# Kernel tuning notes

Measured on AMD Instinct MI355X. Metric: run time of the kernel, lower is better.

Reference implementation:

```python
import jax, jax.numpy as jnp
import numpy as np

NUM_HEADS = 8
EMBED_DIM = 128
TOTAL_TOKENS = 32768  # must be divisible by NUM_HEADS; per-head seq = 4096


def setup_inputs() -> dict:
    key = jax.random.key(0)
    ks = jax.random.split(key, 7)
    E, H, T = EMBED_DIM, NUM_HEADS, TOTAL_TOKENS
    return {
        "query": jax.random.normal(ks[0], (T, E), dtype=jnp.float32),
        "key": jax.random.normal(ks[1], (T, E), dtype=jnp.float32),    # unused by the module
        "value": jax.random.normal(ks[2], (T, E), dtype=jnp.float32),  # unused by the module
        "W_qkv": jax.random.normal(ks[3], (E, 3 * E), dtype=jnp.float32) * (1.0 / np.sqrt(E)),
        "b_qkv": jax.random.normal(ks[4], (3 * E,), dtype=jnp.float32) * 0.02,
        "u_bias": jax.random.normal(ks[5], (H, E), dtype=jnp.float32) * 0.02,
        "v_bias": jax.random.normal(ks[6], (H, E), dtype=jnp.float32) * 0.02,
    }


def reference(query, key, value, W_qkv, b_qkv, u_bias, v_bias):
    H, E = NUM_HEADS, EMBED_DIM
    # Fused QKV projection (torch Linear: x @ W; W stored [in, 3*out] here)
    qkv = query @ W_qkv + b_qkv                      # [T, 3E]
    q, k, v = jnp.split(qkv, 3, axis=-1)             # each [T, E]

    def heads(x):
        # view(-1, H, E).transpose(0, 1): token axis is split across heads
        return jnp.swapaxes(x.reshape(-1, H, E), 0, 1)  # [H, S, E], S = T // H

    q = heads(q) + u_bias[:, None, :]                # per-head additive bias on q
    k = heads(k) + v_bias[:, None, :]                # per-head additive bias on k
    v = heads(v)

    scale = 1.0 / jnp.sqrt(jnp.asarray(E, dtype=q.dtype))
    scores = jnp.einsum('hse,hte->hst', q, k) * scale  # [H, S, S]
    attn = jax.nn.softmax(scores, axis=-1)
    return jnp.einsum('hst,hte->hse', attn, v)         # [H, S, E]
```

## Files before the change

kernel.cpp:

```cpp
#include <hip/hip_runtime.h>
#include <hip/hip_bf16.h>
#include <stdint.h>

#define NHEADS 8
#define SEQ    4096
#define DIM    128
#define TOK    32768

typedef __attribute__((ext_vector_type(4)))  float  f32x4;
typedef __attribute__((ext_vector_type(16))) float  f32x16;
typedef __attribute__((ext_vector_type(8)))  short  bf16x8;
typedef __attribute__((ext_vector_type(8)))  unsigned short u16x8;
typedef __attribute__((ext_vector_type(4)))  unsigned int   u32x4;

__device__ __forceinline__ unsigned short f32_to_bf16(float f) {
  union { float f; unsigned int u; } cv; cv.f = f;
  unsigned int u = cv.u;
  u += 0x7FFFu + ((u >> 16) & 1u);
  return (unsigned short)(u >> 16);
}
__device__ __forceinline__ unsigned cvtpk(float lo, float hi) {
  unsigned r;
  asm("v_cvt_pk_bf16_f32 %0, %1, %2" : "=v"(r) : "v"(lo), "v"(hi));
  return r;
}

__global__ __launch_bounds__(256) void wt_prep_kernel(
    const float* __restrict__ W, unsigned short* __restrict__ Wt) {
  const int tid = threadIdx.x;
  const int j  = blockIdx.x * 32 + (tid >> 3);
  const int k0 = (tid & 7) * 16;
  u16x8 a, b;
  #pragma unroll
  for (int x = 0; x < 8; ++x) a[x] = f32_to_bf16(W[(size_t)(k0 + x) * 384 + j]);
  #pragma unroll
  for (int x = 0; x < 8; ++x) b[x] = f32_to_bf16(W[(size_t)(k0 + 8 + x) * 384 + j]);
  *reinterpret_cast<u16x8*>(Wt + (size_t)j * 128 + k0)     = a;
  *reinterpret_cast<u16x8*>(Wt + (size_t)j * 128 + k0 + 8) = b;
}

__global__ __launch_bounds__(256, 2) void qkv_proj_kernel(
    const float* __restrict__ qin, const unsigned short* __restrict__ Wt,
    const float* __restrict__ bqkv, const float* __restrict__ ubias,
    const float* __restrict__ vbias,
    unsigned short* __restrict__ Qh, unsigned short* __restrict__ Kh,
    unsigned short* __restrict__ Vh) {
  __shared__ __align__(16) char Xl[16384];

  const int tid  = threadIdx.x;
  const int lane = tid & 63;
  const int w    = tid >> 6;
  const int wm   = w & 1;
  const int wn   = w >> 1;
  const int col  = lane & 31;
  const int hi   = lane >> 5;
  const int tok0 = blockIdx.x * 64;

  #pragma unroll
  for (int c = 0; c < 4; ++c) {
    int idx = tid + c * 256;
    int row = idx >> 4, c16 = idx & 15;
    const float* src = qin + (size_t)(tok0 + row) * DIM + c16 * 8;
    f32x4 lo  = *reinterpret_cast<const f32x4*>(src);
    f32x4 hi4 = *reinterpret_cast<const f32x4*>(src + 4);
    u32x4 pk;
    pk[0] = cvtpk(lo[0],  lo[1]);  pk[1] = cvtpk(lo[2],  lo[3]);
    pk[2] = cvtpk(hi4[0], hi4[1]); pk[3] = cvtpk(hi4[2], hi4[3]);
    *reinterpret_cast<u32x4*>(Xl + ((row * 256 + c16 * 16) ^ ((row & 7) << 4))) = pk;
  }
  __syncthreads();

  bf16x8 af[8];
  {
    int row = wm * 32 + col;
    #pragma unroll
    for (int kk = 0; kk < 8; ++kk)
      af[kk] = *reinterpret_cast<const bf16x8*>(
          Xl + ((row * 256 + kk * 32 + hi * 16) ^ ((row & 7) << 4)));
  }

  const int s0 = blockIdx.x * 8 + wm * 4;
  const float scale = 0.1275174309f;

  #pragma unroll
  for (int nt = 0; nt < 6; ++nt) {
    const int j0 = wn * 192 + nt * 32;

    const unsigned short* wp = Wt + (size_t)(j0 + col) * 128 + hi * 8;
    f32x16 acc = (f32x16)(0.0f);
    #pragma unroll
    for (int kk = 0; kk < 8; ++kk) {
      bf16x8 bf = *reinterpret_cast<const bf16x8*>(wp + kk * 16);
      acc = __builtin_amdgcn_mfma_f32_32x32x16_bf16(af[kk], bf, acc, 0, 0, 0);
    }

    const float bqv = bqkv[j0 + col];
    if (j0 < 128) {
      const int e = j0 + col;
      float ub[4];
      #pragma unroll
      for (int r = 0; r < 4; ++r) ub[r] = ubias[(r + 4 * hi) * DIM + e];
      #pragma unroll
      for (int i = 0; i < 16; ++i) {
        int h = (i & 3) + 4 * hi;
        Qh[((size_t)h * SEQ + s0 + (i >> 2)) * DIM + e] =
            f32_to_bf16((acc[i] + bqv + ub[i & 3]) * scale);
      }
    } else if (j0 < 256) {
      const int e = j0 - 128 + col;
      float vb[4];
      #pragma unroll
      for (int r = 0; r < 4; ++r) vb[r] = vbias[(r + 4 * hi) * DIM + e];
      #pragma unroll
      for (int i = 0; i < 16; ++i) {
        int h = (i & 3) + 4 * hi;
        Kh[((size_t)h * SEQ + s0 + (i >> 2)) * DIM + e] =
            f32_to_bf16(acc[i] + bqv + vb[i & 3]);
      }
    } else {
      const int e = j0 - 256 + col;
      #pragma unroll
      for (int i = 0; i < 16; ++i) {
        int h = (i & 3) + 4 * hi;
        Vh[((size_t)h * SEQ + s0 + (i >> 2)) * DIM + e] =
            f32_to_bf16(acc[i] + bqv);
      }
    }
  }
}

__global__ __launch_bounds__(256) void v_transpose_kernel(
    const unsigned short* __restrict__ Vh, unsigned short* __restrict__ Vt) {
  __shared__ unsigned short tile[64][66];
  const int h   = blockIdx.z;
  const int st  = blockIdx.y;
  const int et  = blockIdx.x;
  const int tid = threadIdx.x;

  #pragma unroll
  for (int c = 0; c < 2; ++c) {
    int idx = tid + c * 256;
    int sl  = idx >> 3;
    int e8  = idx & 7;
    u16x8 v = *reinterpret_cast<const u16x8*>(
        Vh + ((size_t)h * SEQ + st * 64 + sl) * DIM + et * 64 + e8 * 8);
    #pragma unroll
    for (int j = 0; j < 8; ++j) tile[sl][e8 * 8 + j] = v[j];
  }
  __syncthreads();
  #pragma unroll
  for (int c = 0; c < 2; ++c) {
    int idx = tid + c * 256;
    int el  = idx >> 3;
    int s8  = idx & 7;
    u16x8 v;
    #pragma unroll
    for (int j = 0; j < 8; ++j) v[j] = tile[s8 * 8 + j][el];
    *reinterpret_cast<u16x8*>(
        Vt + ((size_t)h * DIM + et * 64 + el) * SEQ + st * 64 + s8 * 8) = v;
  }
}

__global__ __launch_bounds__(256, 2) void attn_fwd_kernel(
    const unsigned short* __restrict__ Qh, const unsigned short* __restrict__ Kh,
    const unsigned short* __restrict__ Vt, float* __restrict__ Out) {
  __shared__ __align__(16) char smem[75008];
  float* lbuf = reinterpret_cast<float*>(smem + 73728);
  float* linv = reinterpret_cast<float*>(smem + 74752);

  const int tid  = threadIdx.x;
  const int lane = tid & 63;
  const int w    = tid >> 6;
  const int g    = w >> 1;
  const int wq   = w & 1;
  const int gtid = tid & 127;
  const int col  = lane & 31;
  const int hi   = lane >> 5;
  const int h    = blockIdx.x & 7;
  const int qb   = blockIdx.x >> 3;
  const int q0   = qb * 64 + wq * 32;

  bf16x8 qf[8];
  const unsigned short* qp = Qh + ((size_t)h * SEQ + q0 + col) * DIM + hi * 8;
  #pragma unroll
  for (int kk = 0; kk < 8; ++kk)
    qf[kk] = *reinterpret_cast<const bf16x8*>(qp + kk * 16);

  f32x16 acc[4];
  #pragma unroll
  for (int nt = 0; nt < 4; ++nt) acc[nt] = (f32x16)(0.0f);
  float l_r = 0.0f;

  const unsigned short* Kbase =
      Kh + (size_t)h * SEQ * DIM + (size_t)g * 2048 * DIM;
  const unsigned short* Vbase =
      Vt + (size_t)h * DIM * SEQ + (size_t)g * 2048;

  char* Kg = smem + g * 16384;
  char* Vg = smem + 32768 + g * 20480;

  bf16x8 kr[4], vr[4];

  auto load_tile = [&](int t) {
    #pragma unroll
    for (int c = 0; c < 4; ++c) {
      int idx = gtid + c * 128;
      int row = idx >> 4, c16 = idx & 15;
      kr[c] = *reinterpret_cast<const bf16x8*>(
          Kbase + (size_t)(t * 32 + row) * DIM + c16 * 8);
    }
    #pragma unroll
    for (int c = 0; c < 4; ++c) {
      int idx = gtid + c * 128;
      int e = idx >> 2, c8 = idx & 3;
      vr[c] = *reinterpret_cast<const bf16x8*>(
          Vbase + (size_t)e * SEQ + t * 32 + c8 * 8);
    }
  };
  auto write_tile = [&](int buf) {
    char* KB = Kg + buf * 8192;
    char* VB = Vg + buf * 10240;
    #pragma unroll
    for (int c = 0; c < 4; ++c) {
      int idx = gtid + c * 128;
      int row = idx >> 4, c16 = idx & 15;
      *reinterpret_cast<bf16x8*>(KB + ((row * 256 + c16 * 16) ^ ((row & 7) << 4))) = kr[c];
    }
    #pragma unroll
    for (int c = 0; c < 4; ++c) {
      int idx = gtid + c * 128;
      int e = idx >> 2, c8 = idx & 3;
      *reinterpret_cast<bf16x8*>(VB + (e * 80 + c8 * 16)) = vr[c];
    }
  };

  load_tile(0);
  write_tile(0);
  __syncthreads();

  for (int t = 0; t < 64; ++t) {
    const int cur = t & 1;
    if (t < 63) load_tile(t + 1);

    const char* KB = Kg + cur * 8192;
    const char* VB = Vg + cur * 10240;

    f32x16 sc0 = (f32x16)(0.0f);
    __builtin_amdgcn_s_setprio(1);
    #pragma unroll
    for (int kk = 0; kk < 8; ++kk) {
      bf16x8 kf = *reinterpret_cast<const bf16x8*>(
          KB + ((col * 256 + kk * 32 + hi * 16) ^ ((col & 7) << 4)));
      sc0 = __builtin_amdgcn_mfma_f32_32x32x16_bf16(kf, qf[kk], sc0, 0, 0, 0);
    }
    __builtin_amdgcn_s_setprio(0);

    bf16x8 vf0[2], vf1[2], vf2[2], vf3[2];
    #pragma unroll
    for (int ks = 0; ks < 2; ++ks) {
      vf0[ks] = *reinterpret_cast<const bf16x8*>(VB + ((col) * 80 + ks * 32 + hi * 16));
      vf1[ks] = *reinterpret_cast<const bf16x8*>(VB + ((32 + col) * 80 + ks * 32 + hi * 16));
      vf2[ks] = *reinterpret_cast<const bf16x8*>(VB + ((64 + col) * 80 + ks * 32 + hi * 16));
      vf3[ks] = *reinterpret_cast<const bf16x8*>(VB + ((96 + col) * 80 + ks * 32 + hi * 16));
    }

    float p[16];
    #pragma unroll
    for (int i = 0; i < 16; ++i) {
      p[i] = exp2f(sc0[i] - 16.0f);
      l_r += p[i];
    }
    bf16x8 pa[2];
    #pragma unroll
    for (int s16 = 0; s16 < 2; ++s16) {
      const float* p8 = &p[s16 * 8];
      unsigned A = cvtpk(p8[0], p8[1]);
      unsigned B = cvtpk(p8[4], p8[5]);
      asm("v_permlane32_swap_b32 %0, %1" : "+v"(A), "+v"(B));
      unsigned C = cvtpk(p8[2], p8[3]);
      unsigned D = cvtpk(p8[6], p8[7]);
      asm("v_permlane32_swap_b32 %0, %1" : "+v"(C), "+v"(D));
      u32x4 wd; wd[0] = A; wd[1] = C; wd[2] = B; wd[3] = D;
      pa[s16] = *reinterpret_cast<bf16x8*>(&wd);
    }

    __builtin_amdgcn_s_setprio(1);
    #pragma unroll
    for (int ks = 0; ks < 2; ++ks) {
      acc[0] = __builtin_amdgcn_mfma_f32_32x32x16_bf16(pa[ks], vf0[ks], acc[0], 0, 0, 0);
      acc[1] = __builtin_amdgcn_mfma_f32_32x32x16_bf16(pa[ks], vf1[ks], acc[1], 0, 0, 0);
      acc[2] = __builtin_amdgcn_mfma_f32_32x32x16_bf16(pa[ks], vf2[ks], acc[2], 0, 0, 0);
      acc[3] = __builtin_amdgcn_mfma_f32_32x32x16_bf16(pa[ks], vf3[ks], acc[3], 0, 0, 0);
    }
    __builtin_amdgcn_s_setprio(0);

    if (t < 63) write_tile(cur ^ 1);
    __syncthreads();
  }

  lbuf[w * 64 + lane] = l_r;
  if (g == 1) {
    char* mb = smem + wq * 16384;
    #pragma unroll
    for (int nt = 0; nt < 4; ++nt)
      #pragma unroll
      for (int i = 0; i < 4; ++i) {
        f32x4 v;
        v[0] = acc[nt][4 * i + 0]; v[1] = acc[nt][4 * i + 1];
        v[2] = acc[nt][4 * i + 2]; v[3] = acc[nt][4 * i + 3];
        *reinterpret_cast<f32x4*>(mb + (nt * 4 + i) * 1024 + lane * 16) = v;
      }
  }
  __syncthreads();
  if (g == 0) {
    const char* mb = smem + wq * 16384;
    #pragma unroll
    for (int nt = 0; nt < 4; ++nt)
      #pragma unroll
      for (int i = 0; i < 4; ++i) {
        f32x4 v = *reinterpret_cast<const f32x4*>(mb + (nt * 4 + i) * 1024 + lane * 16);
        acc[nt][4 * i + 0] += v[0]; acc[nt][4 * i + 1] += v[1];
        acc[nt][4 * i + 2] += v[2]; acc[nt][4 * i + 3] += v[3];
      }
    float ltot = lbuf[wq * 64 + col] + lbuf[wq * 64 + col + 32] +
                 lbuf[(wq + 2) * 64 + col] + lbuf[(wq + 2) * 64 + col + 32];
    linv[wq * 32 + col] = 1.0f / ltot;
    asm volatile("s_waitcnt lgkmcnt(0)" ::: "memory");

    float* op = Out + ((size_t)h * SEQ + q0) * DIM + col;
    #pragma unroll
    for (int g2 = 0; g2 < 4; ++g2) {
      f32x4 iv = *reinterpret_cast<f32x4*>(&linv[wq * 32 + 8 * g2 + 4 * hi]);
      #pragma unroll
      for (int nt = 0; nt < 4; ++nt)
        #pragma unroll
        for (int i = 0; i < 4; ++i)
          op[(size_t)(8 * g2 + 4 * hi + i) * DIM + nt * 32] =
              acc[nt][4 * g2 + i] * iv[i];
    }
  }
}

extern "C" void kernel_launch(void* const* d_in, const int* in_sizes, int n_in,
                              void* d_out, int out_size, void* d_ws, size_t ws_size,
                              hipStream_t stream) {
  (void)in_sizes; (void)n_in; (void)out_size; (void)ws_size;
  const float* query = (const float*)d_in[0];
  const float* W_qkv = (const float*)d_in[3];
  const float* b_qkv = (const float*)d_in[4];
  const float* u_bias = (const float*)d_in[5];
  const float* v_bias = (const float*)d_in[6];
  float* out = (float*)d_out;

  const size_t per = (size_t)NHEADS * SEQ * DIM;
  unsigned short* Qh = (unsigned short*)d_ws;
  unsigned short* Kh = Qh + per;
  unsigned short* Vh = Kh + per;
  unsigned short* Vt = Vh + per;
  unsigned short* Wt = Vt;

  wt_prep_kernel<<<dim3(12), dim3(256), 0, stream>>>(W_qkv, Wt);
  qkv_proj_kernel<<<dim3(TOK / 64), dim3(256), 0, stream>>>(
      query, Wt, b_qkv, u_bias, v_bias, Qh, Kh, Vh);
  v_transpose_kernel<<<dim3(2, 64, 8), dim3(256), 0, stream>>>(Vh, Vt);
  attn_fwd_kernel<<<dim3(NHEADS * 64), dim3(256), 0, stream>>>(Qh, Kh, Vt, out);
}
```

Baseline: 139.1 us.

## Use direct global-to-LDS loads and 12-wave blocks with 3-way KV split

The attention kernel now uses 768-thread blocks: 4 query waves (128 queries per block) times 3 KV groups that split the sequence into 43/43/42 tiles. K/V tiles are copied with global_load_lds, which removes the register staging and LDS write pass of the old prefetch. The PV MFMAs are split into two halves to lower register pressure. This brings a 3-way reduction through shared memory, 256 blocks on 256 CUs with one block per CU, and about 134KB of LDS per block. The launch bound of 768 threads with 3 blocks per CU is not reachable with that much LDS.

```diff
diff --git a/kernel.cpp b/kernel.cpp
--- a/kernel.cpp
+++ b/kernel.cpp
@@ -23,6 +23,11 @@
   unsigned r;
   asm("v_cvt_pk_bf16_f32 %0, %1, %2" : "=v"(r) : "v"(lo), "v"(hi));
   return r;
+}
+__device__ __forceinline__ void gload16(const void* g, void* l) {
+  __builtin_amdgcn_global_load_lds(
+      (const __attribute__((address_space(1))) unsigned int*)g,
+      (__attribute__((address_space(3))) unsigned int*)l, 16, 0, 0);
 }
 
 __global__ __launch_bounds__(256) void wt_prep_kernel(
@@ -161,24 +166,29 @@
   }
 }
 
-__global__ __launch_bounds__(256, 2) void attn_fwd_kernel(
+__global__ __launch_bounds__(768, 3) void attn_fwd_kernel(
     const unsigned short* __restrict__ Qh, const unsigned short* __restrict__ Kh,
     const unsigned short* __restrict__ Vt, float* __restrict__ Out) {
-  __shared__ __align__(16) char smem[75008];
-  float* lbuf = reinterpret_cast<float*>(smem + 73728);
-  float* linv = reinterpret_cast<float*>(smem + 74752);
+  __shared__ __align__(16) char smem[134656];
+  float* lbuf = reinterpret_cast<float*>(smem + 131072);
+  float* linv = reinterpret_cast<float*>(smem + 134144);
 
   const int tid  = threadIdx.x;
   const int lane = tid & 63;
   const int w    = tid >> 6;
-  const int g    = w >> 1;
-  const int wq   = w & 1;
-  const int gtid = tid & 127;
+  const int g    = w >> 2;
+  const int wq   = w & 3;
   const int col  = lane & 31;
   const int hi   = lane >> 5;
   const int h    = blockIdx.x & 7;
   const int qb   = blockIdx.x >> 3;
-  const int q0   = qb * 64 + wq * 32;
+  const int q0   = qb * 128 + wq * 32;
+
+  const int tbase = g * 43;
+  const int nt    = (g == 2) ? 42 : 43;
+
+  char* Kg = smem + g * 16384;
+  char* Vg = smem + 49152 + g * 20480;
 
   bf16x8 qf[8];
   const unsigned short* qp = Qh + ((size_t)h * SEQ + q0 + col) * DIM + hi * 8;
@@ -188,142 +198,144 @@
 
   f32x16 acc[4];
   #pragma unroll
-  for (int nt = 0; nt < 4; ++nt) acc[nt] = (f32x16)(0.0f);
+  for (int n = 0; n < 4; ++n) acc[n] = (f32x16)(0.0f);
   float l_r = 0.0f;
 
-  const unsigned short* Kbase =
-      Kh + (size_t)h * SEQ * DIM + (size_t)g * 2048 * DIM;
-  const unsigned short* Vbase =
-      Vt + (size_t)h * DIM * SEQ + (size_t)g * 2048;
-
-  char* Kg = smem + g * 16384;
-  char* Vg = smem + 32768 + g * 20480;
-
-  bf16x8 kr[4], vr[4];
-
-  auto load_tile = [&](int t) {
-    #pragma unroll
-    for (int c = 0; c < 4; ++c) {
-      int idx = gtid + c * 128;
-      int row = idx >> 4, c16 = idx & 15;
-      kr[c] = *reinterpret_cast<const bf16x8*>(
-          Kbase + (size_t)(t * 32 + row) * DIM + c16 * 8);
-    }
-    #pragma unroll
-    for (int c = 0; c < 4; ++c) {
-      int idx = gtid + c * 128;
-      int e = idx >> 2, c8 = idx & 3;
-      vr[c] = *reinterpret_cast<const bf16x8*>(
-          Vbase + (size_t)e * SEQ + t * 32 + c8 * 8);
+  int kofs[2];
+  #pragma unroll
+  for (int c2 = 0; c2 < 2; ++c2) {
+    int c   = wq * 2 + c2;
+    int row = c * 4 + (lane >> 4);
+    kofs[c2] = row * 256 + ((((lane & 15) ^ (row & 7)) << 4));
+  }
+  int vofs[3];
+  #pragma unroll
+  for (int c2 = 0; c2 < 3; ++c2) {
+    int c     = wq + 4 * c2;
+    int laddr = c * 1024 + lane * 16;
+    int row   = laddr / 80;
+    int unit  = (laddr - row * 80) >> 4;
+    vofs[c2]  = row * (SEQ * 2) + (unit < 4 ? unit * 16 : 0);
+  }
+
+  const char* KbaseB = reinterpret_cast<const char*>(Kh + (size_t)h * SEQ * DIM);
+  const char* VbaseB = reinterpret_cast<const char*>(Vt + (size_t)h * DIM * SEQ);
+
+  auto stage = [&](int tl, int buf) {
+    const char* ks = KbaseB + (size_t)(tbase + tl) * 8192;
+    #pragma unroll
+    for (int c2 = 0; c2 < 2; ++c2)
+      gload16(ks + kofs[c2], Kg + buf * 8192 + (wq * 2 + c2) * 1024);
+    const char* vs = VbaseB + (size_t)(tbase + tl) * 64;
+    #pragma unroll
+    for (int c2 = 0; c2 < 3; ++c2) {
+      int c = wq + 4 * c2;
+      if (c < 10)
+        gload16(vs + vofs[c2], Vg + buf * 10240 + c * 1024);
     }
   };
-  auto write_tile = [&](int buf) {
-    char* KB = Kg + buf * 8192;
-    char* VB = Vg + buf * 10240;
-    #pragma unroll
-    for (int c = 0; c < 4; ++c) {
-      int idx = gtid + c * 128;
-      int row = idx >> 4, c16 = idx & 15;
-      *reinterpret_cast<bf16x8*>(KB + ((row * 256 + c16 * 16) ^ ((row & 7) << 4))) = kr[c];
-    }
-    #pragma unroll
-    for (int c = 0; c < 4; ++c) {
-      int idx = gtid + c * 128;
-      int e = idx >> 2, c8 = idx & 3;
-      *reinterpret_cast<bf16x8*>(VB + (e * 80 + c8 * 16)) = vr[c];
-    }
-  };
-
-  load_tile(0);
-  write_tile(0);
+
+  stage(0, 0);
   __syncthreads();
 
-  for (int t = 0; t < 64; ++t) {
-    const int cur = t & 1;
-    if (t < 63) load_tile(t + 1);
-
-    const char* KB = Kg + cur * 8192;
-    const char* VB = Vg + cur * 10240;
-
-    f32x16 sc0 = (f32x16)(0.0f);
-    __builtin_amdgcn_s_setprio(1);
-    #pragma unroll
-    for (int kk = 0; kk < 8; ++kk) {
-      bf16x8 kf = *reinterpret_cast<const bf16x8*>(
-          KB + ((col * 256 + kk * 32 + hi * 16) ^ ((col & 7) << 4)));
-      sc0 = __builtin_amdgcn_mfma_f32_32x32x16_bf16(kf, qf[kk], sc0, 0, 0, 0);
-    }
-    __builtin_amdgcn_s_setprio(0);
-
-    bf16x8 vf0[2], vf1[2], vf2[2], vf3[2];
-    #pragma unroll
-    for (int ks = 0; ks < 2; ++ks) {
-      vf0[ks] = *reinterpret_cast<const bf16x8*>(VB + ((col) * 80 + ks * 32 + hi * 16));
-      vf1[ks] = *reinterpret_cast<const bf16x8*>(VB + ((32 + col) * 80 + ks * 32 + hi * 16));
-      vf2[ks] = *reinterpret_cast<const bf16x8*>(VB + ((64 + col) * 80 + ks * 32 + hi * 16));
-      vf3[ks] = *reinterpret_cast<const bf16x8*>(VB + ((96 + col) * 80 + ks * 32 + hi * 16));
-    }
-
-    float p[16];
-    #pragma unroll
-    for (int i = 0; i < 16; ++i) {
-      p[i] = exp2f(sc0[i] - 16.0f);
-      l_r += p[i];
-    }
-    bf16x8 pa[2];
-    #pragma unroll
-    for (int s16 = 0; s16 < 2; ++s16) {
-      const float* p8 = &p[s16 * 8];
-      unsigned A = cvtpk(p8[0], p8[1]);
-      unsigned B = cvtpk(p8[4], p8[5]);
-      asm("v_permlane32_swap_b32 %0, %1" : "+v"(A), "+v"(B));
-      unsigned C = cvtpk(p8[2], p8[3]);
-      unsigned D = cvtpk(p8[6], p8[7]);
-      asm("v_permlane32_swap_b32 %0, %1" : "+v"(C), "+v"(D));
-      u32x4 wd; wd[0] = A; wd[1] = C; wd[2] = B; wd[3] = D;
-      pa[s16] = *reinterpret_cast<bf16x8*>(&wd);
-    }
-
-    __builtin_amdgcn_s_setprio(1);
-    #pragma unroll
-    for (int ks = 0; ks < 2; ++ks) {
-      acc[0] = __builtin_amdgcn_mfma_f32_32x32x16_bf16(pa[ks], vf0[ks], acc[0], 0, 0, 0);
-      acc[1] = __builtin_amdgcn_mfma_f32_32x32x16_bf16(pa[ks], vf1[ks], acc[1], 0, 0, 0);
-      acc[2] = __builtin_amdgcn_mfma_f32_32x32x16_bf16(pa[ks], vf2[ks], acc[2], 0, 0, 0);
-      acc[3] = __builtin_amdgcn_mfma_f32_32x32x16_bf16(pa[ks], vf3[ks], acc[3], 0, 0, 0);
-    }
-    __builtin_amdgcn_s_setprio(0);
-
-    if (t < 63) write_tile(cur ^ 1);
+  for (int tl = 0; tl < 43; ++tl) {
+    const int cur = tl & 1;
+    if (tl + 1 < nt) stage(tl + 1, cur ^ 1);
+
+    if (tl < nt) {
+      const char* KB = Kg + cur * 8192;
+      const char* VB = Vg + cur * 10240;
+
+      f32x16 sc = (f32x16)(0.0f);
+      __builtin_amdgcn_s_setprio(1);
+      #pragma unroll
+      for (int kk = 0; kk < 8; ++kk) {
+        bf16x8 kf = *reinterpret_cast<const bf16x8*>(
+            KB + ((col * 256 + kk * 32 + hi * 16) ^ ((col & 7) << 4)));
+        sc = __builtin_amdgcn_mfma_f32_32x32x16_bf16(kf, qf[kk], sc, 0, 0, 0);
+      }
+      __builtin_amdgcn_s_setprio(0);
+
+      bf16x8 pa[2];
+      #pragma unroll
+      for (int s16 = 0; s16 < 2; ++s16) {
+        float p8[8];
+        #pragma unroll
+        for (int i = 0; i < 8; ++i) {
+          p8[i] = exp2f(sc[s16 * 8 + i] - 16.0f);
+          l_r += p8[i];
+        }
+        unsigned A = cvtpk(p8[0], p8[1]);
+        unsigned B = cvtpk(p8[4], p8[5]);
+        asm("v_permlane32_swap_b32 %0, %1" : "+v"(A), "+v"(B));
+        unsigned C = cvtpk(p8[2], p8[3]);
+        unsigned D = cvtpk(p8[6], p8[7]);
+        asm("v_permlane32_swap_b32 %0, %1" : "+v"(C), "+v"(D));
+        u32x4 wd; wd[0] = A; wd[1] = C; wd[2] = B; wd[3] = D;
+        pa[s16] = *reinterpret_cast<bf16x8*>(&wd);
+      }
+
+      bf16x8 vf0[2], vf1[2];
+      #pragma unroll
+      for (int ks = 0; ks < 2; ++ks) {
+        vf0[ks] = *reinterpret_cast<const bf16x8*>(VB + (col) * 80 + ks * 32 + hi * 16);
+        vf1[ks] = *reinterpret_cast<const bf16x8*>(VB + (32 + col) * 80 + ks * 32 + hi * 16);
+      }
+      __builtin_amdgcn_s_setprio(1);
+      #pragma unroll
+      for (int ks = 0; ks < 2; ++ks) {
+        acc[0] = __builtin_amdgcn_mfma_f32_32x32x16_bf16(pa[ks], vf0[ks], acc[0], 0, 0, 0);
+        acc[1] = __builtin_amdgcn_mfma_f32_32x32x16_bf16(pa[ks], vf1[ks], acc[1], 0, 0, 0);
+      }
+      __builtin_amdgcn_s_setprio(0);
+      #pragma unroll
+      for (int ks = 0; ks < 2; ++ks) {
+        vf0[ks] = *reinterpret_cast<const bf16x8*>(VB + (64 + col) * 80 + ks * 32 + hi * 16);
+        vf1[ks] = *reinterpret_cast<const bf16x8*>(VB + (96 + col) * 80 + ks * 32 + hi * 16);
+      }
+      __builtin_amdgcn_s_setprio(1);
+      #pragma unroll
+      for (int ks = 0; ks < 2; ++ks) {
+        acc[2] = __builtin_amdgcn_mfma_f32_32x32x16_bf16(pa[ks], vf0[ks], acc[2], 0, 0, 0);
+        acc[3] = __builtin_amdgcn_mfma_f32_32x32x16_bf16(pa[ks], vf1[ks], acc[3], 0, 0, 0);
+      }
+      __builtin_amdgcn_s_setprio(0);
+    }
+
     __syncthreads();
   }
 
   lbuf[w * 64 + lane] = l_r;
-  if (g == 1) {
-    char* mb = smem + wq * 16384;
-    #pragma unroll
-    for (int nt = 0; nt < 4; ++nt)
+  if (g > 0) {
+    char* mb = smem + ((g - 1) * 4 + wq) * 16384;
+    #pragma unroll
+    for (int n = 0; n < 4; ++n)
       #pragma unroll
       for (int i = 0; i < 4; ++i) {
         f32x4 v;
-        v[0] = acc[nt][4 * i + 0]; v[1] = acc[nt][4 * i + 1];
-        v[2] = acc[nt][4 * i + 2]; v[3] = acc[nt][4 * i + 3];
-        *reinterpret_cast<f32x4*>(mb + (nt * 4 + i) * 1024 + lane * 16) = v;
+        v[0] = acc[n][4 * i + 0]; v[1] = acc[n][4 * i + 1];
+        v[2] = acc[n][4 * i + 2]; v[3] = acc[n][4 * i + 3];
+        *reinterpret_cast<f32x4*>(mb + (n * 4 + i) * 1024 + lane * 16) = v;
       }
   }
   __syncthreads();
   if (g == 0) {
-    const char* mb = smem + wq * 16384;
-    #pragma unroll
-    for (int nt = 0; nt < 4; ++nt)
-      #pragma unroll
-      for (int i = 0; i < 4; ++i) {
-        f32x4 v = *reinterpret_cast<const f32x4*>(mb + (nt * 4 + i) * 1024 + lane * 16);
-        acc[nt][4 * i + 0] += v[0]; acc[nt][4 * i + 1] += v[1];
-        acc[nt][4 * i + 2] += v[2]; acc[nt][4 * i + 3] += v[3];
-      }
-    float ltot = lbuf[wq * 64 + col] + lbuf[wq * 64 + col + 32] +
-                 lbuf[(wq + 2) * 64 + col] + lbuf[(wq + 2) * 64 + col + 32];
+    #pragma unroll
+    for (int s = 0; s < 2; ++s) {
+      const char* mb = smem + (s * 4 + wq) * 16384;
+      #pragma unroll
+      for (int n = 0; n < 4; ++n)
+        #pragma unroll
+        for (int i = 0; i < 4; ++i) {
+          f32x4 v = *reinterpret_cast<const f32x4*>(mb + (n * 4 + i) * 1024 + lane * 16);
+          acc[n][4 * i + 0] += v[0]; acc[n][4 * i + 1] += v[1];
+          acc[n][4 * i + 2] += v[2]; acc[n][4 * i + 3] += v[3];
+        }
+    }
+    float ltot = 0.0f;
+    #pragma unroll
+    for (int gg = 0; gg < 3; ++gg)
+      ltot += lbuf[(gg * 4 + wq) * 64 + col] + lbuf[(gg * 4 + wq) * 64 + col + 32];
     linv[wq * 32 + col] = 1.0f / ltot;
     asm volatile("s_waitcnt lgkmcnt(0)" ::: "memory");
 
@@ -332,11 +344,11 @@
     for (int g2 = 0; g2 < 4; ++g2) {
       f32x4 iv = *reinterpret_cast<f32x4*>(&linv[wq * 32 + 8 * g2 + 4 * hi]);
       #pragma unroll
-      for (int nt = 0; nt < 4; ++nt)
+      for (int n = 0; n < 4; ++n)
         #pragma unroll
         for (int i = 0; i < 4; ++i)
-          op[(size_t)(8 * g2 + 4 * hi + i) * DIM + nt * 32] =
-              acc[nt][4 * g2 + i] * iv[i];
+          op[(size_t)(8 * g2 + 4 * hi + i) * DIM + n * 32] =
+              acc[n][4 * g2 + i] * iv[i];
     }
   }
 }
@@ -363,5 +375,5 @@
   qkv_proj_kernel<<<dim3(TOK / 64), dim3(256), 0, stream>>>(
       query, Wt, b_qkv, u_bias, v_bias, Qh, Kh, Vh);
   v_transpose_kernel<<<dim3(2, 64, 8), dim3(256), 0, stream>>>(Vh, Vt);
-  attn_fwd_kernel<<<dim3(NHEADS * 64), dim3(256), 0, stream>>>(Qh, Kh, Vt, out);
-}
+  attn_fwd_kernel<<<dim3(NHEADS * 32), dim3(768), 0, stream>>>(Qh, Kh, Vt, out);
+}
```

Measured after the change: 123.8 us. 1.12x faster.
